# Kernel tuning notes

Measured on AMD Instinct MI355X. Metric: run time of the kernel, lower is better.

## Reference

```python
import jax, jax.numpy as jnp
import numpy as np

D_MODEL = 512
N_HEADS = 8
HEAD_DIM = D_MODEL // N_HEADS
SCALE = float(np.sqrt(HEAD_DIM))


def setup_inputs() -> dict:
    key = jax.random.key(0)
    k1, k2, k3, k4, k5, k6 = jax.random.split(key, 6)
    B, T, S = 4, 2048, 4096
    query = jax.random.normal(k1, (B, T, D_MODEL), dtype=jnp.float32)
    keys = jax.random.normal(k2, (B, S, D_MODEL), dtype=jnp.float32)
    key_padding_mask = jnp.zeros((B, S), dtype=bool)  # all valid
    # Linear params (torch nn.Linear: y = x @ W.T + b)
    lim = 1.0 / np.sqrt(D_MODEL)
    q_w = jax.random.uniform(k3, (D_MODEL, D_MODEL), jnp.float32, -lim, lim)
    q_b = jax.random.uniform(k4, (D_MODEL,), jnp.float32, -lim, lim)
    k_w = jax.random.uniform(k5, (D_MODEL, D_MODEL), jnp.float32, -lim, lim)
    k_b = jax.random.uniform(k6, (D_MODEL,), jnp.float32, -lim, lim)
    return {"query": query, "keys": keys, "key_padding_mask": key_padding_mask,
            "q_w": q_w, "q_b": q_b, "k_w": k_w, "k_b": k_b}


def reference(query, keys, key_padding_mask, q_w, q_b, k_w, k_b):
    B, T, _ = query.shape
    S = keys.shape[1]
    q = (query @ q_w.T + q_b).reshape(B, T, N_HEADS, HEAD_DIM)
    k = (keys @ k_w.T + k_b).reshape(B, S, N_HEADS, HEAD_DIM)
    # mean over heads of scaled per-head QK^T == single contraction over (h,d)
    # divided by n_heads*scale; avoids materializing [B,H,T,S].
    logits = jnp.einsum('bthd,bshd->bts', q, k) / (N_HEADS * SCALE)
    logits = jnp.where(key_padding_mask[:, None, :], -jnp.inf, logits)
    return logits
```

## Files before the change

### kernel.cpp

```cpp
#include <hip/hip_runtime.h>
#include <hip/hip_bf16.h>

using bf16 = __hip_bfloat16;
typedef __attribute__((ext_vector_type(8))) short short8;
typedef __attribute__((ext_vector_type(4))) float floatx4;

#define NEG_INF (-__builtin_huge_valf())

__device__ __forceinline__ void gld_lds16(const void* g, void* l) {
  __builtin_amdgcn_global_load_lds(
      (const __attribute__((address_space(1))) unsigned int*)g,
      (__attribute__((address_space(3))) unsigned int*)l, 16, 0, 0);
}

__global__ void cvt_all(const float* __restrict__ q, const float* __restrict__ k,
                        const float* __restrict__ qw, const float* __restrict__ kw,
                        bf16* __restrict__ qo, bf16* __restrict__ ko,
                        bf16* __restrict__ qwo, bf16* __restrict__ kwo,
                        int nq, int nk, int nw) {
  const long total = ((long)nq + nk + 2L * nw) >> 3;
  for (long i = (long)blockIdx.x * blockDim.x + threadIdx.x; i < total;
       i += (long)gridDim.x * blockDim.x) {
    long e = i << 3;
    const float* src; bf16* dst;
    if (e < nq)                       { src = q  + e;               dst = qo  + e; }
    else if (e < (long)nq + nk)       { src = k  + (e - nq);        dst = ko  + (e - nq); }
    else if (e < (long)nq + nk + nw)  { src = qw + (e - nq - nk);   dst = qwo + (e - nq - nk); }
    else                              { src = kw + (e - nq - nk - nw); dst = kwo + (e - nq - nk - nw); }
    float4 a = *(const float4*)(src);
    float4 b = *(const float4*)(src + 4);
    bf16 t[8];
    t[0] = __float2bfloat16(a.x); t[1] = __float2bfloat16(a.y);
    t[2] = __float2bfloat16(a.z); t[3] = __float2bfloat16(a.w);
    t[4] = __float2bfloat16(b.x); t[5] = __float2bfloat16(b.y);
    t[6] = __float2bfloat16(b.z); t[7] = __float2bfloat16(b.w);
    *(short8*)(dst) = *(short8*)(t);
  }
}

__device__ __forceinline__ void gemm_bt_core(const bf16* __restrict__ A,
                                             const bf16* __restrict__ Bm,
                                             int m0, int n0, int K,
                                             bf16* sA, bf16* sB,
                                             floatx4 acc[4][4]) {
  const int tid  = threadIdx.x;
  const int lane = tid & 63;
  const int w    = tid >> 6;
  const int wm   = (w >> 1) * 64;
  const int wn   = (w & 1) * 64;
  const int st_row = lane >> 2;
  const int st_col = (lane & 3) * 8;
  const int frag_m = lane & 15;
  const int frag_k = (lane >> 4) * 8;

  #pragma unroll
  for (int mi = 0; mi < 4; ++mi)
    #pragma unroll
    for (int ni = 0; ni < 4; ++ni)
      acc[mi][ni] = (floatx4){0.f, 0.f, 0.f, 0.f};

  for (int kt = 0; kt < K; kt += 32) {
    #pragma unroll
    for (int j = 0; j < 2; ++j) {
      const int r = (w << 5) + (j << 4);
      const bf16* ga = A  + (size_t)(m0 + r + st_row) * K + kt + st_col;
      const bf16* gb = Bm + (size_t)(n0 + r + st_row) * K + kt + st_col;
      gld_lds16(ga, sA + r * 32);
      gld_lds16(gb, sB + r * 32);
    }
    __syncthreads();

    short8 af[4], bfv[4];
    const bf16* pa = sA + (wm + frag_m) * 32 + frag_k;
    const bf16* pb = sB + (wn + frag_m) * 32 + frag_k;
    #pragma unroll
    for (int i = 0; i < 4; ++i) af[i]  = *(const short8*)(pa + i * 16 * 32);
    #pragma unroll
    for (int i = 0; i < 4; ++i) bfv[i] = *(const short8*)(pb + i * 16 * 32);
    #pragma unroll
    for (int mi = 0; mi < 4; ++mi)
      #pragma unroll
      for (int ni = 0; ni < 4; ++ni)
        acc[mi][ni] = __builtin_amdgcn_mfma_f32_16x16x32_bf16(af[mi], bfv[ni],
                                                              acc[mi][ni], 0, 0, 0);
    __syncthreads();
  }
}

__global__ __launch_bounds__(256) void proj_gemm(const bf16* __restrict__ A,
                                                 const bf16* __restrict__ W,
                                                 const float* __restrict__ bias,
                                                 bf16* __restrict__ out) {
  __shared__ bf16 sA[128 * 32];
  __shared__ bf16 sB[128 * 32];
  const int m0 = blockIdx.x * 128;
  const int n0 = blockIdx.y * 128;
  floatx4 acc[4][4];
  gemm_bt_core(A, W, m0, n0, 512, sA, sB, acc);

  const int lane = threadIdx.x & 63;
  const int w = threadIdx.x >> 6;
  const int wm = (w >> 1) * 64, wn = (w & 1) * 64;
  const int col = lane & 15;
  const int rbase = (lane >> 4) * 4;
  #pragma unroll
  for (int ni = 0; ni < 4; ++ni) {
    const int gn = n0 + wn + ni * 16 + col;
    const float b = bias[gn];
    #pragma unroll
    for (int mi = 0; mi < 4; ++mi) {
      const int gm = m0 + wm + mi * 16 + rbase;
      #pragma unroll
      for (int r = 0; r < 4; ++r)
        out[(size_t)(gm + r) * 512 + gn] = __float2bfloat16(acc[mi][ni][r] + b);
    }
  }
}

__global__ __launch_bounds__(256) void qk_gemm(const bf16* __restrict__ Q,
                                               const bf16* __restrict__ Kp,
                                               const unsigned char* __restrict__ mask,
                                               float* __restrict__ out) {
  __shared__ bf16 sA[128 * 32];
  __shared__ bf16 sB[128 * 32];
  const int b = blockIdx.z;
  const bf16* A  = Q  + (size_t)b * 2048 * 512;
  const bf16* Bm = Kp + (size_t)b * 4096 * 512;
  float* ob = out + (size_t)b * 2048 * 4096;
  const unsigned char* mb = mask + (size_t)b * 4096;
  const int m0 = blockIdx.x * 128;
  const int n0 = blockIdx.y * 128;
  floatx4 acc[4][4];
  gemm_bt_core(A, Bm, m0, n0, 512, sA, sB, acc);

  const int lane = threadIdx.x & 63;
  const int w = threadIdx.x >> 6;
  const int wm = (w >> 1) * 64, wn = (w & 1) * 64;
  const int col = lane & 15;
  const int rbase = (lane >> 4) * 4;
  const float scale = 1.0f / 64.0f;
  #pragma unroll
  for (int ni = 0; ni < 4; ++ni) {
    const int gn = n0 + wn + ni * 16 + col;
    const bool msk = mb[gn] != 0;
    #pragma unroll
    for (int mi = 0; mi < 4; ++mi) {
      const int gm = m0 + wm + mi * 16 + rbase;
      #pragma unroll
      for (int r = 0; r < 4; ++r)
        ob[(size_t)(gm + r) * 4096 + gn] = msk ? NEG_INF : acc[mi][ni][r] * scale;
    }
  }
}

extern "C" void kernel_launch(void* const* d_in, const int* in_sizes, int n_in,
                              void* d_out, int out_size, void* d_ws, size_t ws_size,
                              hipStream_t stream) {
  const float* query = (const float*)d_in[0];
  const float* keys  = (const float*)d_in[1];
  const unsigned char* mask = (const unsigned char*)d_in[2];
  const float* q_w = (const float*)d_in[3];
  const float* q_b = (const float*)d_in[4];
  const float* k_w = (const float*)d_in[5];
  const float* k_b = (const float*)d_in[6];
  float* out = (float*)d_out;

  const int B = 4, T = 2048, S = 4096, D = 512;
  const int nq = B * T * D;
  const int nk = B * S * D;
  const int nw = D * D;

  char* ws = (char*)d_ws;
  bf16* query_bf = (bf16*)(ws);
  bf16* keys_bf  = (bf16*)(ws + (size_t)nq * 2);
  bf16* qw_bf    = (bf16*)(ws + (size_t)(nq + nk) * 2);
  bf16* kw_bf    = (bf16*)(ws + (size_t)(nq + nk + nw) * 2);
  bf16* q_proj   = (bf16*)(ws + (size_t)(nq + nk + 2 * nw) * 2);
  bf16* k_proj   = (bf16*)(ws + (size_t)(nq + nk + 2 * nw + nq) * 2);

  cvt_all<<<2048, 256, 0, stream>>>(query, keys, q_w, k_w,
                                    query_bf, keys_bf, qw_bf, kw_bf, nq, nk, nw);
  proj_gemm<<<dim3(B * T / 128, D / 128), 256, 0, stream>>>(query_bf, qw_bf, q_b, q_proj);
  proj_gemm<<<dim3(B * S / 128, D / 128), 256, 0, stream>>>(keys_bf, kw_bf, k_b, k_proj);
  qk_gemm<<<dim3(T / 128, S / 128, B), 256, 0, stream>>>(q_proj, k_proj, mask, out);
}
```

Measured before the change: 274.2 us.

## Fuse fp32-to-bf16 conversion into a single merged Q/K projection GEMM

Removes the separate conversion kernel and instead loads fp32 inputs and weights directly in the projection GEMM, converting them to bf16 in registers before writing to shared memory. The Q and K projections are merged into one launch using a block-index split. This drops a full write and re-read of bf16 copies of the inputs plus two kernel launches. In exchange, the projection loads move from direct global-to-LDS transfers to register-staged fp32 loads, and each weight tile is reconverted per block.

Result: faster. 239.7 us (-12.6%).

```diff
diff --git a/kernel.cpp b/kernel.cpp
--- a/kernel.cpp
+++ b/kernel.cpp
@@ -13,36 +13,32 @@
       (__attribute__((address_space(3))) unsigned int*)l, 16, 0, 0);
 }
 
-__global__ void cvt_all(const float* __restrict__ q, const float* __restrict__ k,
-                        const float* __restrict__ qw, const float* __restrict__ kw,
-                        bf16* __restrict__ qo, bf16* __restrict__ ko,
-                        bf16* __restrict__ qwo, bf16* __restrict__ kwo,
-                        int nq, int nk, int nw) {
-  const long total = ((long)nq + nk + 2L * nw) >> 3;
-  for (long i = (long)blockIdx.x * blockDim.x + threadIdx.x; i < total;
-       i += (long)gridDim.x * blockDim.x) {
-    long e = i << 3;
-    const float* src; bf16* dst;
-    if (e < nq)                       { src = q  + e;               dst = qo  + e; }
-    else if (e < (long)nq + nk)       { src = k  + (e - nq);        dst = ko  + (e - nq); }
-    else if (e < (long)nq + nk + nw)  { src = qw + (e - nq - nk);   dst = qwo + (e - nq - nk); }
-    else                              { src = kw + (e - nq - nk - nw); dst = kwo + (e - nq - nk - nw); }
-    float4 a = *(const float4*)(src);
-    float4 b = *(const float4*)(src + 4);
-    bf16 t[8];
-    t[0] = __float2bfloat16(a.x); t[1] = __float2bfloat16(a.y);
-    t[2] = __float2bfloat16(a.z); t[3] = __float2bfloat16(a.w);
-    t[4] = __float2bfloat16(b.x); t[5] = __float2bfloat16(b.y);
-    t[6] = __float2bfloat16(b.z); t[7] = __float2bfloat16(b.w);
-    *(short8*)(dst) = *(short8*)(t);
-  }
-}
-
-__device__ __forceinline__ void gemm_bt_core(const bf16* __restrict__ A,
-                                             const bf16* __restrict__ Bm,
-                                             int m0, int n0, int K,
-                                             bf16* sA, bf16* sB,
-                                             floatx4 acc[4][4]) {
+__device__ __forceinline__ void cvt8(const float4& a, const float4& b, bf16* t) {
+  t[0] = __float2bfloat16(a.x); t[1] = __float2bfloat16(a.y);
+  t[2] = __float2bfloat16(a.z); t[3] = __float2bfloat16(a.w);
+  t[4] = __float2bfloat16(b.x); t[5] = __float2bfloat16(b.y);
+  t[6] = __float2bfloat16(b.z); t[7] = __float2bfloat16(b.w);
+}
+
+__global__ __launch_bounds__(256) void proj_fused(const float* __restrict__ X,
+                                                  const float* __restrict__ Y,
+                                                  const float* __restrict__ qw,
+                                                  const float* __restrict__ kw,
+                                                  const float* __restrict__ qb,
+                                                  const float* __restrict__ kb,
+                                                  bf16* __restrict__ qo,
+                                                  bf16* __restrict__ ko) {
+  __shared__ bf16 sA[128 * 32];
+  __shared__ bf16 sB[128 * 32];
+  const int mt = blockIdx.x;
+  const bool isQ = mt < 64;
+  const float* A    = isQ ? X  : Y;
+  const float* W    = isQ ? qw : kw;
+  const float* bias = isQ ? qb : kb;
+  bf16* out         = isQ ? qo : ko;
+  const int m0 = (isQ ? mt : mt - 64) * 128;
+  const int n0 = blockIdx.y * 128;
+
   const int tid  = threadIdx.x;
   const int lane = tid & 63;
   const int w    = tid >> 6;
@@ -53,20 +49,29 @@
   const int frag_m = lane & 15;
   const int frag_k = (lane >> 4) * 8;
 
+  floatx4 acc[4][4];
   #pragma unroll
   for (int mi = 0; mi < 4; ++mi)
     #pragma unroll
     for (int ni = 0; ni < 4; ++ni)
       acc[mi][ni] = (floatx4){0.f, 0.f, 0.f, 0.f};
 
-  for (int kt = 0; kt < K; kt += 32) {
+  for (int kt = 0; kt < 512; kt += 32) {
     #pragma unroll
     for (int j = 0; j < 2; ++j) {
       const int r = (w << 5) + (j << 4);
-      const bf16* ga = A  + (size_t)(m0 + r + st_row) * K + kt + st_col;
-      const bf16* gb = Bm + (size_t)(n0 + r + st_row) * K + kt + st_col;
-      gld_lds16(ga, sA + r * 32);
-      gld_lds16(gb, sB + r * 32);
+      const int row = r + st_row;
+      const float* ga = A + (size_t)(m0 + row) * 512 + kt + st_col;
+      const float* gb = W + (size_t)(n0 + row) * 512 + kt + st_col;
+      float4 a0 = *(const float4*)ga;
+      float4 a1 = *(const float4*)(ga + 4);
+      float4 b0 = *(const float4*)gb;
+      float4 b1 = *(const float4*)(gb + 4);
+      bf16 ta[8], tb[8];
+      cvt8(a0, a1, ta);
+      cvt8(b0, b1, tb);
+      *(short8*)(sA + row * 32 + st_col) = *(short8*)ta;
+      *(short8*)(sB + row * 32 + st_col) = *(short8*)tb;
     }
     __syncthreads();
 
@@ -85,22 +90,7 @@
                                                               acc[mi][ni], 0, 0, 0);
     __syncthreads();
   }
-}
-
-__global__ __launch_bounds__(256) void proj_gemm(const bf16* __restrict__ A,
-                                                 const bf16* __restrict__ W,
-                                                 const float* __restrict__ bias,
-                                                 bf16* __restrict__ out) {
-  __shared__ bf16 sA[128 * 32];
-  __shared__ bf16 sB[128 * 32];
-  const int m0 = blockIdx.x * 128;
-  const int n0 = blockIdx.y * 128;
-  floatx4 acc[4][4];
-  gemm_bt_core(A, W, m0, n0, 512, sA, sB, acc);
-
-  const int lane = threadIdx.x & 63;
-  const int w = threadIdx.x >> 6;
-  const int wm = (w >> 1) * 64, wn = (w & 1) * 64;
+
   const int col = lane & 15;
   const int rbase = (lane >> 4) * 4;
   #pragma unroll
@@ -130,12 +120,51 @@
   const unsigned char* mb = mask + (size_t)b * 4096;
   const int m0 = blockIdx.x * 128;
   const int n0 = blockIdx.y * 128;
+
+  const int tid  = threadIdx.x;
+  const int lane = tid & 63;
+  const int w    = tid >> 6;
+  const int wm   = (w >> 1) * 64;
+  const int wn   = (w & 1) * 64;
+  const int st_row = lane >> 2;
+  const int st_col = (lane & 3) * 8;
+  const int frag_m = lane & 15;
+  const int frag_k = (lane >> 4) * 8;
+
   floatx4 acc[4][4];
-  gemm_bt_core(A, Bm, m0, n0, 512, sA, sB, acc);
-
-  const int lane = threadIdx.x & 63;
-  const int w = threadIdx.x >> 6;
-  const int wm = (w >> 1) * 64, wn = (w & 1) * 64;
+  #pragma unroll
+  for (int mi = 0; mi < 4; ++mi)
+    #pragma unroll
+    for (int ni = 0; ni < 4; ++ni)
+      acc[mi][ni] = (floatx4){0.f, 0.f, 0.f, 0.f};
+
+  for (int kt = 0; kt < 512; kt += 32) {
+    #pragma unroll
+    for (int j = 0; j < 2; ++j) {
+      const int r = (w << 5) + (j << 4);
+      const bf16* ga = A  + (size_t)(m0 + r + st_row) * 512 + kt + st_col;
+      const bf16* gb = Bm + (size_t)(n0 + r + st_row) * 512 + kt + st_col;
+      gld_lds16(ga, sA + r * 32);
+      gld_lds16(gb, sB + r * 32);
+    }
+    __syncthreads();
+
+    short8 af[4], bfv[4];
+    const bf16* pa = sA + (wm + frag_m) * 32 + frag_k;
+    const bf16* pb = sB + (wn + frag_m) * 32 + frag_k;
+    #pragma unroll
+    for (int i = 0; i < 4; ++i) af[i]  = *(const short8*)(pa + i * 16 * 32);
+    #pragma unroll
+    for (int i = 0; i < 4; ++i) bfv[i] = *(const short8*)(pb + i * 16 * 32);
+    #pragma unroll
+    for (int mi = 0; mi < 4; ++mi)
+      #pragma unroll
+      for (int ni = 0; ni < 4; ++ni)
+        acc[mi][ni] = __builtin_amdgcn_mfma_f32_16x16x32_bf16(af[mi], bfv[ni],
+                                                              acc[mi][ni], 0, 0, 0);
+    __syncthreads();
+  }
+
   const int col = lane & 15;
   const int rbase = (lane >> 4) * 4;
   const float scale = 1.0f / 64.0f;
@@ -168,19 +197,12 @@
   const int B = 4, T = 2048, S = 4096, D = 512;
   const int nq = B * T * D;
   const int nk = B * S * D;
-  const int nw = D * D;
 
   char* ws = (char*)d_ws;
-  bf16* query_bf = (bf16*)(ws);
-  bf16* keys_bf  = (bf16*)(ws + (size_t)nq * 2);
-  bf16* qw_bf    = (bf16*)(ws + (size_t)(nq + nk) * 2);
-  bf16* kw_bf    = (bf16*)(ws + (size_t)(nq + nk + nw) * 2);
-  bf16* q_proj   = (bf16*)(ws + (size_t)(nq + nk + 2 * nw) * 2);
-  bf16* k_proj   = (bf16*)(ws + (size_t)(nq + nk + 2 * nw + nq) * 2);
-
-  cvt_all<<<2048, 256, 0, stream>>>(query, keys, q_w, k_w,
-                                    query_bf, keys_bf, qw_bf, kw_bf, nq, nk, nw);
-  proj_gemm<<<dim3(B * T / 128, D / 128), 256, 0, stream>>>(query_bf, qw_bf, q_b, q_proj);
-  proj_gemm<<<dim3(B * S / 128, D / 128), 256, 0, stream>>>(keys_bf, kw_bf, k_b, k_proj);
+  bf16* q_proj = (bf16*)(ws);
+  bf16* k_proj = (bf16*)(ws + (size_t)nq * 2);
+
+  proj_fused<<<dim3(192, D / 128), 256, 0, stream>>>(query, keys, q_w, k_w,
+                                                     q_b, k_b, q_proj, k_proj);
   qk_gemm<<<dim3(T / 128, S / 128, B), 256, 0, stream>>>(q_proj, k_proj, mask, out);
 }
```
